# Optimization experiments

Hardware: AMD Instinct MI355X
Metric: run time of the kernel (lower is better)

The kernel has to match this reference:

```python
import jax, jax.numpy as jnp
import numpy as np

N = 40000       # nodes
DEG = 16        # in-degree per node (self-constructed so in_deg > 0)
E = N * DEG     # edges
DIN = 128       # in_ent_feats == out_ent_feats
H = 8           # num_heads
D = DIN // H    # head_dim = 16
FF = 4 * DIN    # FFN hidden
HOPS = 5
ALPHA = 0.15
EPS = 1e-5


def _ln(x, g, b):
    m = jnp.mean(x, axis=-1, keepdims=True)
    v = jnp.mean((x - m) ** 2, axis=-1, keepdims=True)
    return (x - m) / jnp.sqrt(v + EPS) * g + b


def setup_inputs() -> dict:
    key = jax.random.key(0)
    ks = jax.random.split(key, 12)
    s = 0.05
    feat = jax.random.normal(ks[0], (N, DIN), dtype=jnp.float32)
    src = jax.random.randint(ks[1], (E,), 0, N, dtype=jnp.int32)
    # every node gets exactly DEG incoming edges -> in_degree > 0 everywhere
    dst = jnp.repeat(jnp.arange(N, dtype=jnp.int32), DEG)
    return {
        "feat": feat,
        "Wh": jax.random.normal(ks[2], (DIN, DIN), dtype=jnp.float32) * s,
        "Wt": jax.random.normal(ks[3], (DIN, DIN), dtype=jnp.float32) * s,
        "We": jax.random.normal(ks[4], (DIN, DIN), dtype=jnp.float32) * s,
        "attn_p": jax.random.normal(ks[5], (H, D), dtype=jnp.float32) * s,
        "g_head": jax.random.normal(ks[6], (H, D), dtype=jnp.float32) * s,
        "g_tail": jax.random.normal(ks[7], (H, D), dtype=jnp.float32) * s,
        "ln1_g": jnp.ones((DIN,), jnp.float32),
        "ln1_b": jnp.zeros((DIN,), jnp.float32),
        "ln2_g": jnp.ones((DIN,), jnp.float32),
        "ln2_b": jnp.zeros((DIN,), jnp.float32),
        "W1": jax.random.normal(ks[8], (FF, DIN), dtype=jnp.float32) * s,
        "b1": jnp.zeros((FF,), jnp.float32),
        "W2": jax.random.normal(ks[9], (DIN, FF), dtype=jnp.float32) * s,
        "b2": jnp.zeros((DIN,), jnp.float32),
        "src": src,
        "dst": dst,
    }


def reference(feat, Wh, Wt, We, attn_p, g_head, g_tail, ln1_g, ln1_b,
              ln2_g, ln2_b, W1, b1, W2, b2, src, dst):
    n = feat.shape[0]
    h = _ln(feat, ln1_g, ln1_b)                      # feat_drop is identity (eval)
    fh = (h @ Wh.T).reshape(n, H, D)                 # feat_head
    ft = (h @ Wt.T).reshape(n, H, D)                 # feat_tail
    fe = (h @ We.T).reshape(n, H, D)                 # feat_enti ('ft' in dgl)

    # attention logits: (u_mul_v . attn).sum(-1) / head_dim, scaled by log(in_deg) of dst
    e = jnp.sum(fh[src] * ft[dst] * attn_p, axis=-1) / D          # [E, H]
    in_deg = jax.ops.segment_sum(jnp.ones_like(dst, jnp.float32), dst, num_segments=n)
    log_in = jnp.log(in_deg)                                       # [N]
    e = e * log_in[dst][:, None]

    # gate scores
    gh = jnp.sum(fh * g_head, axis=-1)                             # [N, H]
    gt = jnp.sum(ft * g_tail, axis=-1)
    gate = jax.nn.sigmoid(gh[src] + gt[dst])                       # [E, H]

    # weighted edge softmax (per-dst stabilized, gated)
    mx = jax.ops.segment_max(e, dst, num_segments=n)               # [N, H]
    tag = jnp.exp(e - mx[dst]) * gate
    ssum = jax.ops.segment_sum(tag, dst, num_segments=n)
    a = tag / ssum[dst]                                            # [E, H]

    # PPR diffusion
    feat0 = fe
    f = feat0
    for _ in range(HOPS):
        msg = f[src] * a[..., None]                                # [E, H, D]
        agg = jax.ops.segment_sum(msg, dst, num_segments=n)
        f = (1.0 - ALPHA) * agg + ALPHA * feat0

    # residual (Identity since in == out), flatten, FFN block
    rst = (f + feat.reshape(n, H, D)).reshape(n, -1)               # [N, DIN]
    x = _ln(rst, ln2_g, ln2_b)
    ff = jax.nn.relu(x @ W1.T + b1) @ W2.T + b2
    return ff + rst
```

## Files before the change

kernel.cpp:

```cpp
#include <hip/hip_runtime.h>
#include <math.h>

#define N_NODES 40000
#define DEG 16
#define DIN 128
#define NH 8
#define DH 16
#define FFDIM 512
#define ALPHA 0.15f
#define LNEPS 1e-5f

typedef __attribute__((ext_vector_type(8))) short bf16x8;
typedef __attribute__((ext_vector_type(4))) float f32x4;
typedef __attribute__((ext_vector_type(4))) unsigned int u32x4;

__device__ inline unsigned int f2bf(float f) {
    unsigned int u = __float_as_uint(f);
    return (u + 0x7fffu + ((u >> 16) & 1u)) >> 16;
}
__device__ inline float bflo(unsigned u) { return __uint_as_float(u << 16); }
__device__ inline float bfhi(unsigned u) { return __uint_as_float(u & 0xffff0000u); }

__device__ inline float wave_sum64(float v) {
#pragma unroll
    for (int m = 32; m >= 1; m >>= 1) v += __shfl_xor(v, m, 64);
    return v;
}

__global__ void cvt_weights(const float* __restrict__ wh, const float* __restrict__ wt,
                            const float* __restrict__ we, const float* __restrict__ w1,
                            const float* __restrict__ w2,
                            short* __restrict__ owh, short* __restrict__ owt,
                            short* __restrict__ owe, short* __restrict__ ow1,
                            short* __restrict__ ow2) {
    int i = blockIdx.x * 256 + threadIdx.x;
    if (i < 16384)       owh[i]          = (short)f2bf(wh[i]);
    else if (i < 32768)  owt[i - 16384]  = (short)f2bf(wt[i - 16384]);
    else if (i < 49152)  owe[i - 32768]  = (short)f2bf(we[i - 32768]);
    else if (i < 114688) ow1[i - 49152]  = (short)f2bf(w1[i - 49152]);
    else if (i < 180224) ow2[i - 114688] = (short)f2bf(w2[i - 114688]);
}

__global__ void ln_kernel(const float* __restrict__ in, const float* __restrict__ g,
                          const float* __restrict__ b, short* __restrict__ out, int n) {
    int wid  = (blockIdx.x * blockDim.x + threadIdx.x) >> 6;
    int lane = threadIdx.x & 63;
    if (wid >= n) return;
    float2 v = *(const float2*)(in + (size_t)wid * DIN + lane * 2);
    float mean = wave_sum64(v.x + v.y) * (1.0f / DIN);
    float dx = v.x - mean, dy = v.y - mean;
    float var = wave_sum64(dx * dx + dy * dy) * (1.0f / DIN);
    float rstd = rsqrtf(var + LNEPS);
    float2 gg = *(const float2*)(g + lane * 2);
    float2 bb = *(const float2*)(b + lane * 2);
    float o0 = dx * rstd * gg.x + bb.x, o1 = dy * rstd * gg.y + bb.y;
    unsigned int pack = f2bf(o0) | (f2bf(o1) << 16);
    *(unsigned int*)(out + (size_t)wid * DIN + lane * 2) = pack;
}

__global__ void add_ln_kernel(const short* __restrict__ fT, const float* __restrict__ feat,
                              const float* __restrict__ g, const float* __restrict__ b,
                              float* __restrict__ rst, short* __restrict__ x, int n) {
    int wid  = (blockIdx.x * blockDim.x + threadIdx.x) >> 6;
    int lane = threadIdx.x & 63;
    if (wid >= n) return;
    int h = lane >> 3, d2 = (lane & 7) * 2;
    unsigned uf = *(const unsigned*)(fT + ((size_t)h * N_NODES + wid) * 16 + d2);
    float2 va = { bflo(uf), bfhi(uf) };
    float2 vb = *(const float2*)(feat + (size_t)wid * DIN + lane * 2);
    float2 r = { va.x + vb.x, va.y + vb.y };
    *(float2*)(rst + (size_t)wid * DIN + lane * 2) = r;
    float mean = wave_sum64(r.x + r.y) * (1.0f / DIN);
    float dx = r.x - mean, dy = r.y - mean;
    float var = wave_sum64(dx * dx + dy * dy) * (1.0f / DIN);
    float rstd = rsqrtf(var + LNEPS);
    float2 gg = *(const float2*)(g + lane * 2);
    float2 bb = *(const float2*)(b + lane * 2);
    float o0 = dx * rstd * gg.x + bb.x, o1 = dy * rstd * gg.y + bb.y;
    unsigned int pack = f2bf(o0) | (f2bf(o1) << 16);
    *(unsigned int*)(x + (size_t)wid * DIN + lane * 2) = pack;
}

__global__ __launch_bounds__(256) void mfma_gemm(
        const short* __restrict__ A, const short* __restrict__ B,
        int M, int N, int K,
        const float* __restrict__ bias, const float* __restrict__ res, int relu, int tmode,
        float* __restrict__ Cf, short* __restrict__ Cb) {
    __shared__ __align__(16) short Al[64 * 64];
    __shared__ __align__(16) short Bl[128 * 64];
    const int t  = threadIdx.x;
    const int bm = blockIdx.x * 64;
    const int bn = blockIdx.y * 128;
    const int w = t >> 6, lane = t & 63;
    const int wr = w >> 1, wc = w & 1;
    const int l15 = lane & 15, l4 = lane >> 4;
    f32x4 acc[2][4] = {};
    for (int k0 = 0; k0 < K; k0 += 64) {
        __syncthreads();
#pragma unroll
        for (int q = 0; q < 2; ++q) {
            int c = t + q * 256;
            int r = c >> 3, kb = c & 7;
            bf16x8 v = *(const bf16x8*)(A + (size_t)(bm + r) * K + k0 + kb * 8);
            *(bf16x8*)(Al + (r * 8 + (kb ^ (r & 7))) * 8) = v;
        }
#pragma unroll
        for (int q = 0; q < 4; ++q) {
            int c = t + q * 256;
            int r = c >> 3, kb = c & 7;
            bf16x8 v = *(const bf16x8*)(B + (size_t)(bn + r) * K + k0 + kb * 8);
            *(bf16x8*)(Bl + (r * 8 + (kb ^ (r & 7))) * 8) = v;
        }
        __syncthreads();
#pragma unroll
        for (int kc = 0; kc < 2; ++kc) {
            bf16x8 af[2], bfr[4];
#pragma unroll
            for (int mf = 0; mf < 2; ++mf) {
                int row = wr * 32 + mf * 16 + l15;
                int kb = kc * 4 + l4;
                af[mf] = *(const bf16x8*)(Al + (row * 8 + (kb ^ (row & 7))) * 8);
            }
#pragma unroll
            for (int nf = 0; nf < 4; ++nf) {
                int row = wc * 64 + nf * 16 + l15;
                int kb = kc * 4 + l4;
                bfr[nf] = *(const bf16x8*)(Bl + (row * 8 + (kb ^ (row & 7))) * 8);
            }
#pragma unroll
            for (int mf = 0; mf < 2; ++mf)
#pragma unroll
                for (int nf = 0; nf < 4; ++nf)
                    acc[mf][nf] = __builtin_amdgcn_mfma_f32_16x16x32_bf16(
                        af[mf], bfr[nf], acc[mf][nf], 0, 0, 0);
        }
    }
#pragma unroll
    for (int mf = 0; mf < 2; ++mf) {
#pragma unroll
        for (int nf = 0; nf < 4; ++nf) {
            int gcol = bn + wc * 64 + nf * 16 + l15;
            float bv = bias ? bias[gcol] : 0.f;
#pragma unroll
            for (int r = 0; r < 4; ++r) {
                int grow = bm + wr * 32 + mf * 16 + l4 * 4 + r;
                float v = acc[mf][nf][r] + bv;
                if (relu) v = fmaxf(v, 0.f);
                if (tmode) {
                    size_t toff = ((size_t)(gcol >> 4) * M + grow) * 16 + (gcol & 15);
                    Cb[toff] = (short)f2bf(v);
                } else {
                    size_t off = (size_t)grow * N + gcol;
                    if (res) v += res[off];
                    if (Cb) Cb[off] = (short)f2bf(v);
                    if (Cf) Cf[off] = v;
                }
            }
        }
    }
}

__global__ void gates_kernel(const short* __restrict__ fhT, const short* __restrict__ ftT,
                             const float* __restrict__ g_head, const float* __restrict__ g_tail,
                             float* __restrict__ ghT, float* __restrict__ gtT, int total) {
    int t = blockIdx.x * blockDim.x + threadIdx.x;
    if (t >= total) return;
    int h = t / N_NODES;
    const float* gp = g_head + h * DH;
    const float* gq = g_tail + h * DH;
    const short* fp = fhT + (size_t)t * 16;
    const short* fq = ftT + (size_t)t * 16;
    float s1 = 0.f, s2 = 0.f;
#pragma unroll
    for (int d = 0; d < DH; d += 2) {
        unsigned a = *(const unsigned*)(fp + d);
        unsigned b = *(const unsigned*)(fq + d);
        s1 += bflo(a) * gp[d] + bfhi(a) * gp[d + 1];
        s2 += bflo(b) * gq[d] + bfhi(b) * gq[d + 1];
    }
    ghT[t] = s1;
    gtT[t] = s2;
}

__global__ __launch_bounds__(256) void attn_kernel(
        const short* __restrict__ fhT, const short* __restrict__ ftT,
        const float* __restrict__ ghT, const float* __restrict__ gtT,
        const float* __restrict__ attn_p, const int* __restrict__ src,
        short* __restrict__ avT) {
    int h = blockIdx.x & 7;
    int chunk = blockIdx.x >> 3;
    int wv = threadIdx.x >> 6, lane = threadIdx.x & 63;
    int node = chunk * 64 + wv * 16 + (lane >> 2);
    int egrp = lane & 3;
    const size_t hb = (size_t)h * N_NODES;
    const short* tp = ftT + (hb + node) * 16;
    u32x4 ta = *(const u32x4*)tp;
    u32x4 tb = *(const u32x4*)(tp + 8);
    const float* p = attn_p + h * DH;
    const float c = 0.17328679513998632f;
    float q[16];
#pragma unroll
    for (int k = 0; k < 4; ++k) {
        q[2 * k]     = bflo(ta[k]) * p[2 * k] * c;
        q[2 * k + 1] = bfhi(ta[k]) * p[2 * k + 1] * c;
        q[8 + 2 * k]     = bflo(tb[k]) * p[8 + 2 * k] * c;
        q[8 + 2 * k + 1] = bfhi(tb[k]) * p[8 + 2 * k + 1] * c;
    }
    float gtv = gtT[hb + node];
    int4 s4 = *(const int4*)(src + node * DEG + egrp * 4);
    int ss[4] = { s4.x, s4.y, s4.z, s4.w };
    float lg[4], gg[4];
#pragma unroll
    for (int j = 0; j < 4; ++j) {
        const short* fr = fhT + (hb + ss[j]) * 16;
        u32x4 a = *(const u32x4*)fr;
        u32x4 b = *(const u32x4*)(fr + 8);
        float s = 0.f;
#pragma unroll
        for (int k = 0; k < 4; ++k) {
            s += q[2 * k] * bflo(a[k]) + q[2 * k + 1] * bfhi(a[k]);
            s += q[8 + 2 * k] * bflo(b[k]) + q[8 + 2 * k + 1] * bfhi(b[k]);
        }
        lg[j] = s;
        gg[j] = ghT[hb + ss[j]];
    }
    float m = fmaxf(fmaxf(lg[0], lg[1]), fmaxf(lg[2], lg[3]));
    m = fmaxf(m, __shfl_xor(m, 1, 64));
    m = fmaxf(m, __shfl_xor(m, 2, 64));
    float tv[4], sum = 0.f;
#pragma unroll
    for (int j = 0; j < 4; ++j) {
        float gate = 1.f / (1.f + expf(-(gg[j] + gtv)));
        tv[j] = expf(lg[j] - m) * gate;
        sum += tv[j];
    }
    sum += __shfl_xor(sum, 1, 64);
    sum += __shfl_xor(sum, 2, 64);
    float inv = 1.f / sum;
    unsigned pk0 = f2bf(tv[0] * inv) | (f2bf(tv[1] * inv) << 16);
    unsigned pk1 = f2bf(tv[2] * inv) | (f2bf(tv[3] * inv) << 16);
    unsigned* ao = (unsigned*)(avT + (hb + node) * 16 + egrp * 4);
    ao[0] = pk0;
    ao[1] = pk1;
}

__global__ __launch_bounds__(256) void hop_kernel(
        const short* __restrict__ finT, const short* __restrict__ feT,
        const short* __restrict__ avT, const int* __restrict__ src,
        short* __restrict__ foutT) {
    int h = blockIdx.x & 7;
    int chunk = blockIdx.x >> 3;
    int wv = threadIdx.x >> 6, lane = threadIdx.x & 63;
    int node = chunk * 64 + wv * 16 + (lane >> 2);
    int egrp = lane & 3;
    const size_t hb = (size_t)h * N_NODES;
    int4 s4 = *(const int4*)(src + node * DEG + egrp * 4);
    int ss[4] = { s4.x, s4.y, s4.z, s4.w };
    const short* ap = avT + (hb + node) * 16 + egrp * 4;
    unsigned aw0 = *(const unsigned*)(ap);
    unsigned aw1 = *(const unsigned*)(ap + 2);
    float w[4] = { bflo(aw0), bfhi(aw0), bflo(aw1), bfhi(aw1) };
    float acc[16] = {};
#pragma unroll
    for (int j = 0; j < 4; ++j) {
        const short* fr = finT + (hb + ss[j]) * 16;
        u32x4 a = *(const u32x4*)fr;
        u32x4 b = *(const u32x4*)(fr + 8);
#pragma unroll
        for (int k = 0; k < 4; ++k) {
            acc[2 * k]     += w[j] * bflo(a[k]);
            acc[2 * k + 1] += w[j] * bfhi(a[k]);
            acc[8 + 2 * k]     += w[j] * bflo(b[k]);
            acc[8 + 2 * k + 1] += w[j] * bfhi(b[k]);
        }
    }
#pragma unroll
    for (int k = 0; k < 16; ++k) {
        acc[k] += __shfl_xor(acc[k], 1, 64);
        acc[k] += __shfl_xor(acc[k], 2, 64);
    }
    if (egrp == 0) {
        const short* fp = feT + (hb + node) * 16;
        u32x4 fa = *(const u32x4*)fp;
        u32x4 fb = *(const u32x4*)(fp + 8);
        unsigned pk[8];
#pragma unroll
        for (int k = 0; k < 4; ++k) {
            float o0 = (1.f - ALPHA) * acc[2 * k]     + ALPHA * bflo(fa[k]);
            float o1 = (1.f - ALPHA) * acc[2 * k + 1] + ALPHA * bfhi(fa[k]);
            pk[k] = f2bf(o0) | (f2bf(o1) << 16);
            float o2 = (1.f - ALPHA) * acc[8 + 2 * k]     + ALPHA * bflo(fb[k]);
            float o3 = (1.f - ALPHA) * acc[8 + 2 * k + 1] + ALPHA * bfhi(fb[k]);
            pk[4 + k] = f2bf(o2) | (f2bf(o3) << 16);
        }
        u32x4* op = (u32x4*)(foutT + (hb + node) * 16);
        op[0] = *(u32x4*)pk;
        op[1] = *(u32x4*)(pk + 4);
    }
}

extern "C" void kernel_launch(void* const* d_in, const int* in_sizes, int n_in,
                              void* d_out, int out_size, void* d_ws, size_t ws_size,
                              hipStream_t stream) {
    const float* feat   = (const float*)d_in[0];
    const float* Wh     = (const float*)d_in[1];
    const float* Wt     = (const float*)d_in[2];
    const float* We     = (const float*)d_in[3];
    const float* attn_p = (const float*)d_in[4];
    const float* g_head = (const float*)d_in[5];
    const float* g_tail = (const float*)d_in[6];
    const float* ln1_g  = (const float*)d_in[7];
    const float* ln1_b  = (const float*)d_in[8];
    const float* ln2_g  = (const float*)d_in[9];
    const float* ln2_b  = (const float*)d_in[10];
    const float* W1     = (const float*)d_in[11];
    const float* b1     = (const float*)d_in[12];
    const float* W2     = (const float*)d_in[13];
    const float* b2     = (const float*)d_in[14];
    const int*   src    = (const int*)d_in[15];

    float* ws = (float*)d_ws;
    short* avT = (short*)ws;
    short* feT = (short*)(ws + 2560000);
    float* ghT = ws + 5120000;
    float* gtT = ws + 5440000;
    short* h_bf = (short*)(ws + 5760000);
    short* fhT = (short*)(ws + 8320000);
    short* ftT = (short*)(ws + 10880000);
    short* f0T = (short*)(ws + 13440000);
    short* f1T = (short*)(ws + 16000000);
    short* x_bf = (short*)(ws + 18560000);
    short* wb   = (short*)(ws + 21120000);
    short* wh_bf = wb, *wt_bf = wb + 16384, *we_bf = wb + 32768;
    short* w1_bf = wb + 49152, *w2_bf = wb + 114688;
    short* hidden = (short*)ws;
    float* rst = (float*)d_out;

    dim3 b256(256);
    int nodeBlocks = (N_NODES * 64) / 256;
    int headBlocks = 8 * (N_NODES / 64);

    cvt_weights<<<704, b256, 0, stream>>>(Wh, Wt, We, W1, W2, wh_bf, wt_bf, we_bf, w1_bf, w2_bf);
    ln_kernel<<<nodeBlocks, b256, 0, stream>>>(feat, ln1_g, ln1_b, h_bf, N_NODES);

    dim3 gp(N_NODES / 64, 1);
    mfma_gemm<<<gp, b256, 0, stream>>>(h_bf, wh_bf, N_NODES, DIN, DIN, nullptr, nullptr, 0, 1, nullptr, fhT);
    mfma_gemm<<<gp, b256, 0, stream>>>(h_bf, wt_bf, N_NODES, DIN, DIN, nullptr, nullptr, 0, 1, nullptr, ftT);
    mfma_gemm<<<gp, b256, 0, stream>>>(h_bf, we_bf, N_NODES, DIN, DIN, nullptr, nullptr, 0, 1, nullptr, feT);

    gates_kernel<<<(N_NODES * NH) / 256, b256, 0, stream>>>(fhT, ftT, g_head, g_tail, ghT, gtT, N_NODES * NH);
    attn_kernel<<<headBlocks, b256, 0, stream>>>(fhT, ftT, ghT, gtT, attn_p, src, avT);

    hop_kernel<<<headBlocks, b256, 0, stream>>>(feT, feT, avT, src, f0T);
    hop_kernel<<<headBlocks, b256, 0, stream>>>(f0T, feT, avT, src, f1T);
    hop_kernel<<<headBlocks, b256, 0, stream>>>(f1T, feT, avT, src, f0T);
    hop_kernel<<<headBlocks, b256, 0, stream>>>(f0T, feT, avT, src, f1T);
    hop_kernel<<<headBlocks, b256, 0, stream>>>(f1T, feT, avT, src, f0T);

    add_ln_kernel<<<nodeBlocks, b256, 0, stream>>>(f0T, feat, ln2_g, ln2_b, rst, x_bf, N_NODES);

    dim3 gff1(N_NODES / 64, FFDIM / 128);
    mfma_gemm<<<gff1, b256, 0, stream>>>(x_bf, w1_bf, N_NODES, FFDIM, DIN, b1, nullptr, 1, 0, nullptr, hidden);
    dim3 gff2(N_NODES / 64, 1);
    mfma_gemm<<<gff2, b256, 0, stream>>>(hidden, w2_bf, N_NODES, DIN, FFDIM, b2, rst, 0, 0, rst, nullptr);
}
```

Before: 393.9 us.

## Merge three projection GEMMs into one launch and use nontemporal gather loads

```diff
diff --git a/kernel.cpp b/kernel.cpp
--- a/kernel.cpp
+++ b/kernel.cpp
@@ -20,6 +20,13 @@
 }
 __device__ inline float bflo(unsigned u) { return __uint_as_float(u << 16); }
 __device__ inline float bfhi(unsigned u) { return __uint_as_float(u & 0xffff0000u); }
+
+__device__ inline u32x4 nt16(const short* p) {
+    return __builtin_nontemporal_load((const u32x4*)p);
+}
+__device__ inline float ntf(const float* p) {
+    return __builtin_nontemporal_load(p);
+}
 
 __device__ inline float wave_sum64(float v) {
 #pragma unroll
@@ -160,6 +167,76 @@
     }
 }
 
+__global__ __launch_bounds__(256) void proj3_gemm(
+        const short* __restrict__ A,
+        const short* __restrict__ W0, const short* __restrict__ W1w, const short* __restrict__ W2w,
+        short* __restrict__ C0, short* __restrict__ C1c, short* __restrict__ C2c, int M) {
+    __shared__ __align__(16) short Al[64 * 64];
+    __shared__ __align__(16) short Bl[128 * 64];
+    const int sel = blockIdx.y;
+    const short* B = (sel == 0) ? W0 : (sel == 1) ? W1w : W2w;
+    short* C       = (sel == 0) ? C0 : (sel == 1) ? C1c : C2c;
+    const int t  = threadIdx.x;
+    const int bm = blockIdx.x * 64;
+    const int w = t >> 6, lane = t & 63;
+    const int wr = w >> 1, wc = w & 1;
+    const int l15 = lane & 15, l4 = lane >> 4;
+    f32x4 acc[2][4] = {};
+    for (int k0 = 0; k0 < DIN; k0 += 64) {
+        __syncthreads();
+#pragma unroll
+        for (int q = 0; q < 2; ++q) {
+            int c = t + q * 256;
+            int r = c >> 3, kb = c & 7;
+            bf16x8 v = *(const bf16x8*)(A + (size_t)(bm + r) * DIN + k0 + kb * 8);
+            *(bf16x8*)(Al + (r * 8 + (kb ^ (r & 7))) * 8) = v;
+        }
+#pragma unroll
+        for (int q = 0; q < 4; ++q) {
+            int c = t + q * 256;
+            int r = c >> 3, kb = c & 7;
+            bf16x8 v = *(const bf16x8*)(B + (size_t)r * DIN + k0 + kb * 8);
+            *(bf16x8*)(Bl + (r * 8 + (kb ^ (r & 7))) * 8) = v;
+        }
+        __syncthreads();
+#pragma unroll
+        for (int kc = 0; kc < 2; ++kc) {
+            bf16x8 af[2], bfr[4];
+#pragma unroll
+            for (int mf = 0; mf < 2; ++mf) {
+                int row = wr * 32 + mf * 16 + l15;
+                int kb = kc * 4 + l4;
+                af[mf] = *(const bf16x8*)(Al + (row * 8 + (kb ^ (row & 7))) * 8);
+            }
+#pragma unroll
+            for (int nf = 0; nf < 4; ++nf) {
+                int row = wc * 64 + nf * 16 + l15;
+                int kb = kc * 4 + l4;
+                bfr[nf] = *(const bf16x8*)(Bl + (row * 8 + (kb ^ (row & 7))) * 8);
+            }
+#pragma unroll
+            for (int mf = 0; mf < 2; ++mf)
+#pragma unroll
+                for (int nf = 0; nf < 4; ++nf)
+                    acc[mf][nf] = __builtin_amdgcn_mfma_f32_16x16x32_bf16(
+                        af[mf], bfr[nf], acc[mf][nf], 0, 0, 0);
+        }
+    }
+#pragma unroll
+    for (int mf = 0; mf < 2; ++mf) {
+#pragma unroll
+        for (int nf = 0; nf < 4; ++nf) {
+            int gcol = wc * 64 + nf * 16 + l15;
+#pragma unroll
+            for (int r = 0; r < 4; ++r) {
+                int grow = bm + wr * 32 + mf * 16 + l4 * 4 + r;
+                size_t toff = ((size_t)(gcol >> 4) * M + grow) * 16 + (gcol & 15);
+                C[toff] = (short)f2bf(acc[mf][nf][r]);
+            }
+        }
+    }
+}
+
 __global__ void gates_kernel(const short* __restrict__ fhT, const short* __restrict__ ftT,
                              const float* __restrict__ g_head, const float* __restrict__ g_tail,
                              float* __restrict__ ghT, float* __restrict__ gtT, int total) {
@@ -213,8 +290,8 @@
 #pragma unroll
     for (int j = 0; j < 4; ++j) {
         const short* fr = fhT + (hb + ss[j]) * 16;
-        u32x4 a = *(const u32x4*)fr;
-        u32x4 b = *(const u32x4*)(fr + 8);
+        u32x4 a = nt16(fr);
+        u32x4 b = nt16(fr + 8);
         float s = 0.f;
 #pragma unroll
         for (int k = 0; k < 4; ++k) {
@@ -222,7 +299,7 @@
             s += q[8 + 2 * k] * bflo(b[k]) + q[8 + 2 * k + 1] * bfhi(b[k]);
         }
         lg[j] = s;
-        gg[j] = ghT[hb + ss[j]];
+        gg[j] = ntf(ghT + hb + ss[j]);
     }
     float m = fmaxf(fmaxf(lg[0], lg[1]), fmaxf(lg[2], lg[3]));
     m = fmaxf(m, __shfl_xor(m, 1, 64));
@@ -264,8 +341,8 @@
 #pragma unroll
     for (int j = 0; j < 4; ++j) {
         const short* fr = finT + (hb + ss[j]) * 16;
-        u32x4 a = *(const u32x4*)fr;
-        u32x4 b = *(const u32x4*)(fr + 8);
+        u32x4 a = nt16(fr);
+        u32x4 b = nt16(fr + 8);
 #pragma unroll
         for (int k = 0; k < 4; ++k) {
             acc[2 * k]     += w[j] * bflo(a[k]);
@@ -281,8 +358,8 @@
     }
     if (egrp == 0) {
         const short* fp = feT + (hb + node) * 16;
-        u32x4 fa = *(const u32x4*)fp;
-        u32x4 fb = *(const u32x4*)(fp + 8);
+        u32x4 fa = nt16(fp);
+        u32x4 fb = nt16(fp + 8);
         unsigned pk[8];
 #pragma unroll
         for (int k = 0; k < 4; ++k) {
@@ -343,10 +420,8 @@
     cvt_weights<<<704, b256, 0, stream>>>(Wh, Wt, We, W1, W2, wh_bf, wt_bf, we_bf, w1_bf, w2_bf);
     ln_kernel<<<nodeBlocks, b256, 0, stream>>>(feat, ln1_g, ln1_b, h_bf, N_NODES);
 
-    dim3 gp(N_NODES / 64, 1);
-    mfma_gemm<<<gp, b256, 0, stream>>>(h_bf, wh_bf, N_NODES, DIN, DIN, nullptr, nullptr, 0, 1, nullptr, fhT);
-    mfma_gemm<<<gp, b256, 0, stream>>>(h_bf, wt_bf, N_NODES, DIN, DIN, nullptr, nullptr, 0, 1, nullptr, ftT);
-    mfma_gemm<<<gp, b256, 0, stream>>>(h_bf, we_bf, N_NODES, DIN, DIN, nullptr, nullptr, 0, 1, nullptr, feT);
+    dim3 gproj(N_NODES / 64, 3);
+    proj3_gemm<<<gproj, b256, 0, stream>>>(h_bf, wh_bf, wt_bf, we_bf, fhT, ftT, feT, N_NODES);
 
     gates_kernel<<<(N_NODES * NH) / 256, b256, 0, stream>>>(fhT, ftT, g_head, g_tail, ghT, gtT, N_NODES * NH);
     attn_kernel<<<headBlocks, b256, 0, stream>>>(fhT, ftT, ghT, gtT, attn_p, src, avT);
```

New measurement: 774.4 us. 96.6% more time.
